# Performance work log

Hardware: AMD Instinct MI355X
Metric: run time of the kernel (lower is better)

The kernel has to match this reference:

```python
import jax, jax.numpy as jnp
import numpy as np

N, K, B, D, H = 256, 128, 256, 256, 512  # code length, info bits, batch, embed dim, MLP hidden


def _mlp(x, W1, b1, W2, b2):
    return jnp.maximum(x @ W1 + b1, 0.0) @ W2 + b2


def setup_inputs():
    key = jax.random.key(0)
    ks = jax.random.split(key, 12)
    perm = np.random.RandomState(0).permutation(N)
    info_set = jnp.sort(jnp.asarray(perm[:K], dtype=jnp.int32))  # unique sorted info positions
    info_bits = jax.random.randint(ks[0], (B, K), 0, 2, dtype=jnp.int32)
    rv = jax.random.uniform(ks[1], (B, N), dtype=jnp.float32)  # one uniform per leaf (sampling)

    def w(k, shape, fan):
        return jax.random.normal(k, shape, jnp.float32) / np.float32(np.sqrt(fan))

    return {
        'info_bits': info_bits,
        'rv': rv,
        'info_set': info_set,
        'obs_emb': w(ks[2], (3, D), D),
        'label_emb': w(ks[3], (3, D), D),
        'cn_W1': w(ks[4], (2 * D, H), 2 * D), 'cn_b1': jnp.zeros((H,), jnp.float32),
        'cn_W2': w(ks[5], (H, D), H), 'cn_b2': jnp.zeros((D,), jnp.float32),
        'bn_W1': w(ks[6], (3 * D, H), 3 * D), 'bn_b1': jnp.zeros((H,), jnp.float32),
        'bn_W2': w(ks[7], (H, D), H), 'bn_b2': jnp.zeros((D,), jnp.float32),
        'llr_W': w(ks[8], (D, 2), D), 'llr_b': jnp.zeros((2,), jnp.float32),
    }


def reference(info_bits, rv, info_set, obs_emb, label_emb,
              cn_W1, cn_b1, cn_W2, cn_b2, bn_W1, bn_b1, bn_W2, bn_b2, llr_W, llr_b):
    batch = info_bits.shape[0]

    def encode(e, f, off, n):
        # e: (B, n, D) float embeddings; f: (B, n, 1) int32 bits (2 == unknown -> sample)
        if n == 1:
            p_uy = jax.nn.softmax(e @ llr_W + llr_b, axis=-1)        # (B, 1, 2) probs
            r = rv[:, off:off + 1]                                    # (B, 1)
            # rv > cdf[...,0] == rv > p(u=0): sample a hard bit
            hard = (r > p_uy[..., 0]).astype(jnp.int32)[..., None]    # (B, 1, 1)
            x = jnp.where(f == 2, hard, f)
            return x, x, p_uy
        half = n // 2
        e_odd, e_even = e[:, ::2], e[:, 1::2]                         # SplitEvenOdd(axis=1)
        f_left, f_right = f[:, :half], f[:, half:]
        u1est = _mlp(jnp.concatenate([e_odd, e_even], -1), cn_W1, cn_b1, cn_W2, cn_b2)
        u1, h1, p_left = encode(u1est, f_left, off, half)
        u_emb = label_emb[h1[..., 0]]                                 # (B, half, D)
        u2est = _mlp(jnp.concatenate([e_odd, e_even, u_emb], -1), bn_W1, bn_b1, bn_W2, bn_b2)
        u2, h2, p_right = encode(u2est, f_right, off + half, half)
        u = jnp.concatenate([u1, u2], 1)
        p_uy = jnp.concatenate([p_left, p_right], 1)
        v_xor = jnp.mod(h1 + h2, 2)
        # Interleave(axis=1): out[::2] = v_xor, out[1::2] = h2
        x = jnp.stack([v_xor, h2], axis=2).reshape(batch, n, 1)
        return u, x, p_uy

    # scatter info bits into the length-N frame (frozen positions stay == 2)
    u_ = jnp.full((batch, N), 2, jnp.int32).at[:, info_set].set(info_bits)
    f = u_[..., None]
    # embedding_observations_nn(2 * ones): embedding of token '2' everywhere
    e = jnp.broadcast_to(obs_emb[2], (batch, N, D))
    u, x, p_u = encode(e, f, 0, N)
    # f: sampled frame with info positions re-masked to 2
    f_out = u[..., 0].at[:, info_set].set(2)[..., None]
    return x, f_out, u, p_u
```

## Files before the change

kernel.cpp:

```cpp
#include <hip/hip_runtime.h>
#include <math.h>

#define NB 256
#define NN 256
#define NK 128
#define ND 256
#define NH 512
#define NT 1024

#define OUT_X 0
#define OUT_F 65536
#define OUT_U 131072
#define OUT_P 196608

#define EPB   65280
#define SP6O  EPB
#define S1O   (SP6O + 1024)
#define S2O   (S1O + 512)
#define S3O   (S2O + 1024)
#define LOFFI (S3O + 2048)
#define BPB   (LOFFI + 256)

__host__ __device__ __forceinline__ int loff(int d) { return 256 - (1 << (9 - d)); }

template <int PC>
__device__ void g1ks(const float* __restrict__ Abuf, float* __restrict__ part,
                     const int tid, const float* __restrict__ W1) {
  const int q = tid >> 8;
  const int c0 = (tid & 255) << 1;
  const float* Wp = W1 + (size_t)(q * 128) * NH + c0;
  const float* Ar = Abuf + q * 128;
  float a0[PC], a1[PC];
#pragma unroll
  for (int r = 0; r < PC; ++r) { a0[r] = 0.f; a1[r] = 0.f; }
  float2 n0 = *(const float2*)Wp;
  float2 n1 = *(const float2*)(Wp + NH);
  float2 n2 = *(const float2*)(Wp + 2 * NH);
  float2 n3 = *(const float2*)(Wp + 3 * NH);
#pragma unroll 2
  for (int kc = 0; kc < 124; kc += 4) {
    const float2 w0 = n0, w1 = n1, w2 = n2, w3 = n3;
    const float* Wn = Wp + (size_t)(kc + 4) * NH;
    n0 = *(const float2*)Wn;
    n1 = *(const float2*)(Wn + NH);
    n2 = *(const float2*)(Wn + 2 * NH);
    n3 = *(const float2*)(Wn + 3 * NH);
#pragma unroll
    for (int r = 0; r < PC; ++r) {
      const float4 av = *(const float4*)(Ar + r * 512 + kc);
      a0[r] += av.x * w0.x + av.y * w1.x + av.z * w2.x + av.w * w3.x;
      a1[r] += av.x * w0.y + av.y * w1.y + av.z * w2.y + av.w * w3.y;
    }
  }
#pragma unroll
  for (int r = 0; r < PC; ++r) {
    const float4 av = *(const float4*)(Ar + r * 512 + 124);
    a0[r] += av.x * n0.x + av.y * n1.x + av.z * n2.x + av.w * n3.x;
    a1[r] += av.x * n0.y + av.y * n1.y + av.z * n2.y + av.w * n3.y;
  }
#pragma unroll
  for (int r = 0; r < PC; ++r)
    *(float2*)&part[(q * PC + r) * 512 + c0] = make_float2(a0[r], a1[r]);
}

template <int PC>
__device__ void g1red(const float* __restrict__ part, float* __restrict__ hid,
                      const int tid, const float* __restrict__ b1,
                      const int isBn, const float* __restrict__ embS,
                      const int* __restrict__ bitR) {
  for (int i = tid; i < PC * 256; i += NT) {
    const int r = i >> 8, c0 = (i & 255) << 1;
    float2 s = *(const float2*)(b1 + c0);
#pragma unroll
    for (int qq = 0; qq < 4; ++qq) {
      const float2 p = *(const float2*)&part[(qq * PC + r) * 512 + c0];
      s.x += p.x; s.y += p.y;
    }
    if (isBn) {
      const float2 e = *(const float2*)&embS[bitR[r] * 512 + c0];
      s.x += e.x; s.y += e.y;
    }
    *(float2*)&hid[r * 512 + c0] = make_float2(fmaxf(s.x, 0.f), fmaxf(s.y, 0.f));
  }
}

template <int R>
__device__ void g1redspec(const float* __restrict__ part, float* __restrict__ hid,
                          const int base, const int tid,
                          const float* __restrict__ b1,
                          const float* __restrict__ embS) {
  for (int i = tid; i < R * 256; i += NT) {
    const int r = i >> 8, c0 = (i & 255) << 1;
    float2 s = *(const float2*)(b1 + c0);
#pragma unroll
    for (int qq = 0; qq < 4; ++qq) {
      const float2 p = *(const float2*)&part[(qq * R + r) * 512 + c0];
      s.x += p.x; s.y += p.y;
    }
    const float2 e0 = *(const float2*)&embS[c0];
    const float2 e1 = *(const float2*)&embS[512 + c0];
    *(float2*)&hid[(base + 2 * r) * 512 + c0] =
        make_float2(fmaxf(s.x + e0.x, 0.f), fmaxf(s.y + e0.y, 0.f));
    *(float2*)&hid[(base + 2 * r + 1) * 512 + c0] =
        make_float2(fmaxf(s.x + e1.x, 0.f), fmaxf(s.y + e1.y, 0.f));
  }
}

template <int RT>
__device__ void g2ks(const float* __restrict__ hid, const int hidBase,
                     float* __restrict__ part, const int tid,
                     const float* __restrict__ W2) {
  const int q = tid >> 7;
  const int c0 = (tid & 127) << 1;
  const float* Wp = W2 + (size_t)(q * 64) * ND + c0;
  const float* Hr = hid + hidBase * 512 + q * 64;
  float a0[RT], a1[RT];
#pragma unroll
  for (int r = 0; r < RT; ++r) { a0[r] = 0.f; a1[r] = 0.f; }
  float2 n0 = *(const float2*)Wp;
  float2 n1 = *(const float2*)(Wp + ND);
  float2 n2 = *(const float2*)(Wp + 2 * ND);
  float2 n3 = *(const float2*)(Wp + 3 * ND);
#pragma unroll 2
  for (int kc = 0; kc < 60; kc += 4) {
    const float2 w0 = n0, w1 = n1, w2 = n2, w3 = n3;
    const float* Wn = Wp + (size_t)(kc + 4) * ND;
    n0 = *(const float2*)Wn;
    n1 = *(const float2*)(Wn + ND);
    n2 = *(const float2*)(Wn + 2 * ND);
    n3 = *(const float2*)(Wn + 3 * ND);
#pragma unroll
    for (int r = 0; r < RT; ++r) {
      const float4 av = *(const float4*)(Hr + r * 512 + kc);
      a0[r] += av.x * w0.x + av.y * w1.x + av.z * w2.x + av.w * w3.x;
      a1[r] += av.x * w0.y + av.y * w1.y + av.z * w2.y + av.w * w3.y;
    }
  }
#pragma unroll
  for (int r = 0; r < RT; ++r) {
    const float4 av = *(const float4*)(Hr + r * 512 + 60);
    a0[r] += av.x * n0.x + av.y * n1.x + av.z * n2.x + av.w * n3.x;
    a1[r] += av.x * n0.y + av.y * n1.y + av.z * n2.y + av.w * n3.y;
  }
#pragma unroll
  for (int r = 0; r < RT; ++r)
    *(float2*)&part[(q * RT + r) * 256 + c0] = make_float2(a0[r], a1[r]);
}

template <int RT>
__device__ void g2red(const float* __restrict__ part, const int tid,
                      const float* __restrict__ b2,
                      float* const* __restrict__ rowDst) {
  for (int i = tid; i < RT * 128; i += NT) {
    const int r = i >> 7, c0 = (i & 127) << 1;
    float2 s = *(const float2*)(b2 + c0);
#pragma unroll
    for (int qq = 0; qq < 8; ++qq) {
      const float2 p = *(const float2*)&part[(qq * RT + r) * 256 + c0];
      s.x += p.x; s.y += p.y;
    }
    *(float2*)(rowDst[r] + c0) = s;
  }
}

__global__ __launch_bounds__(NT, 4) void sc_quad(
    const int* __restrict__ info_bits, const float* __restrict__ rv,
    const int* __restrict__ info_set,
    const float* __restrict__ obs_emb, const float* __restrict__ label_emb,
    const float* __restrict__ cnW1, const float* __restrict__ cnb1,
    const float* __restrict__ cnW2, const float* __restrict__ cnb2,
    const float* __restrict__ bnW1, const float* __restrict__ bnb1,
    const float* __restrict__ bnW2, const float* __restrict__ bnb2,
    const float* __restrict__ llrW, const float* __restrict__ llrb,
    float* __restrict__ out, float* __restrict__ ws) {
  __shared__ float A[4096];
  __shared__ float part[20480];
  __shared__ float hid[8192];
  __shared__ float embS[1024];
  __shared__ float* rowDst[16];
  __shared__ int fmap[256];
  __shared__ int curS[256], nxtS[256];
  __shared__ float red[8];
  __shared__ int bitR[8];
  __shared__ int qbS[4];

  const int tid = threadIdx.x, b = blockIdx.x;
  float* wsb = ws + (size_t)b * BPB;
  float* E = wsb;
  float* sp6 = wsb + SP6O;
  float* S1 = wsb + S1O;
  float* S2 = wsb + S2O;
  float* S3 = wsb + S3O;
  int* Lb = (int*)(wsb + LOFFI);
  const float* obs2 = obs_emb + 2 * ND;

  {
    const int bit = tid >> 9, col = tid & 511;
    float s = 0.f;
#pragma unroll 4
    for (int j = 0; j < ND; ++j)
      s += label_emb[bit * ND + j] * bnW1[(size_t)(NH + j) * NH + col];
    embS[bit * 512 + col] = s;
  }
  if (tid < 256) fmap[tid] = -1;
  __syncthreads();
  if (tid < NK) fmap[info_set[tid]] = tid;
  __syncthreads();

  auto stageA = [&](const float* Ed, int p0, int R) {
    const int n4 = R * 128;
    float4* A4 = (float4*)A;
    if (Ed) {
      const float4* s4 = (const float4*)(Ed + (size_t)(2 * p0) * ND);
      for (int i = tid; i < n4; i += NT) A4[i] = s4[i];
    } else {
      const float4* o4 = (const float4*)obs2;
      for (int i = tid; i < n4; i += NT) A4[i] = o4[i & 63];
    }
  };

  auto plainPass = [&](int d, int isBn) {
    const int P = 1 << (7 - d);
    const float* W1 = isBn ? bnW1 : cnW1;
    const float* B1 = isBn ? bnb1 : cnb1;
    const float* W2 = isBn ? bnW2 : cnW2;
    const float* B2 = isBn ? bnb2 : cnb2;
    const float* Ed = (d == 0) ? nullptr : E + (size_t)loff(d) * ND;
    float* dstE = E + (size_t)loff(d + 1) * ND;
    const int PC = P >= 8 ? 8 : 4;
    for (int p0 = 0; p0 < P; p0 += PC) {
      stageA(Ed, p0, PC);
      if (isBn && tid < PC) bitR[tid] = Lb[loff(d + 1) + p0 + tid];
      if (tid < PC) rowDst[tid] = dstE + (size_t)(p0 + tid) * ND;
      __syncthreads();
      if (PC == 8) {
        g1ks<8>(A, part, tid, W1); __syncthreads();
        g1red<8>(part, hid, tid, B1, isBn, embS, bitR); __syncthreads();
        g2ks<8>(hid, 0, part, tid, W2); __syncthreads();
        g2red<8>(part, tid, B2, rowDst); __syncthreads();
      } else {
        g1ks<4>(A, part, tid, W1); __syncthreads();
        g1red<4>(part, hid, tid, B1, isBn, embS, bitR); __syncthreads();
        g2ks<4>(hid, 0, part, tid, W2); __syncthreads();
        g2red<4>(part, tid, B2, rowDst); __syncthreads();
      }
    }
  };

  auto pair6 = [&]() {
    stageA(E + (size_t)loff(6) * ND, 0, 2);
    if (tid < 2) rowDst[tid] = E + (size_t)(252 + tid) * ND;
    __syncthreads();
    g1ks<2>(A, part, tid, cnW1); __syncthreads();
    g1red<2>(part, hid, tid, cnb1, 0, embS, bitR); __syncthreads();
    g2ks<2>(hid, 0, part, tid, cnW2); __syncthreads();
    g2red<2>(part, tid, cnb2, rowDst); __syncthreads();
    g1ks<2>(A, part, tid, bnW1); __syncthreads();
    g1redspec<2>(part, hid, 2, tid, bnb1, embS); __syncthreads();
    g2ks<4>(hid, 2, part, tid, bnW2);
    if (tid < 4) rowDst[tid] = sp6 + (size_t)tid * ND;
    __syncthreads();
    g2red<4>(part, tid, bnb2, rowDst); __syncthreads();
  };

  auto comb = [&]() {
    for (int i = tid; i < 5 * 128; i += NT) {
      const int r = i >> 7, k = (i & 127) << 2;
      const int h = k >> 8;
      const float* src;
      if (r == 0) src = E + (size_t)(252 + h) * ND;
      else {
        const int cc = r - 1;
        const int bit = (h == 0) ? (cc >> 1) : (cc & 1);
        src = sp6 + (size_t)(h * 2 + bit) * ND;
      }
      *(float4*)&A[r * 512 + k] = *(const float4*)&src[k & 255];
    }
    __syncthreads();
    g1ks<5>(A, part, tid, cnW1); __syncthreads();
    g1red<5>(part, hid, tid, cnb1, 0, embS, bitR); __syncthreads();
    g2ks<5>(hid, 0, part, tid, cnW2);
    if (tid < 5) rowDst[tid] = (tid == 0) ? (E + (size_t)254 * ND)
                                          : (S2 + (size_t)(tid - 1) * ND);
    __syncthreads();
    g2red<5>(part, tid, cnb2, rowDst); __syncthreads();
    g1ks<5>(A, part, tid, bnW1); __syncthreads();
    g1redspec<5>(part, hid, 5, tid, bnb1, embS); __syncthreads();
    g2ks<10>(hid, 5, part, tid, bnW2);
    if (tid < 10) rowDst[tid] = (tid < 2) ? (S1 + (size_t)tid * ND)
                                          : (S3 + (size_t)(tid - 2) * ND);
    __syncthreads();
    g2red<10>(part, tid, bnb2, rowDst); __syncthreads();
  };

  auto leaf = [&](int off) {
    const int ph = off & 3;
    const float* src;
    if (ph == 0) src = E + (size_t)254 * ND;
    else if (ph == 1) src = S1 + (size_t)qbS[0] * ND;
    else {
      const int cidx = 2 * (qbS[0] ^ qbS[1]) + qbS[1];
      src = (ph == 2) ? (S2 + (size_t)cidx * ND)
                      : (S3 + (size_t)(2 * cidx + qbS[2]) * ND);
    }
    if (tid < 256) {
      const float ev = src[tid];
      float v0 = ev * llrW[2 * tid];
      float v1 = ev * llrW[2 * tid + 1];
#pragma unroll
      for (int o = 32; o > 0; o >>= 1) {
        v0 += __shfl_down(v0, o);
        v1 += __shfl_down(v1, o);
      }
      if ((tid & 63) == 0) {
        red[tid >> 6] = v0;
        red[4 + (tid >> 6)] = v1;
      }
    }
    __syncthreads();
    if (tid == 0) {
      const float l0 = red[0] + red[1] + red[2] + red[3] + llrb[0];
      const float l1 = red[4] + red[5] + red[6] + red[7] + llrb[1];
      const float m = fmaxf(l0, l1);
      const float e0 = expf(l0 - m), e1 = expf(l1 - m);
      const float s = e0 + e1;
      const float p0 = e0 / s, p1 = e1 / s;
      const int hard = (rv[b * NN + off] > p0) ? 1 : 0;
      const int fidx = fmap[off];
      const int fval = (fidx >= 0) ? info_bits[b * NK + fidx] : 2;
      const int xb = (fval == 2) ? hard : fval;
      out[OUT_F + b * NN + off] = (fidx >= 0) ? 2.0f : (float)xb;
      out[OUT_U + b * NN + off] = (float)xb;
      out[OUT_P + (b * NN + off) * 2 + 0] = p0;
      out[OUT_P + (b * NN + off) * 2 + 1] = p1;
      curS[0] = xb;
      qbS[ph] = xb;
    }
    __syncthreads();
    int* cur = curS;
    int* nxt = nxtS;
    int len = 1, lev = 8, idx = off;
    while (idx & 1) {
      if (tid < len) {
        const int c = cur[tid];
        nxt[2 * tid] = Lb[loff(lev) + tid] ^ c;
        nxt[2 * tid + 1] = c;
      }
      __syncthreads();
      int* t = cur; cur = nxt; nxt = t;
      len <<= 1; idx >>= 1; --lev;
    }
    if (lev > 0) {
      if (tid < len) Lb[loff(lev) + tid] = cur[tid];
    } else {
      if (tid < 256) out[OUT_X + b * NN + tid] = (float)cur[tid];
    }
    __syncthreads();
  };

  for (int d = 0; d <= 5; ++d) plainPass(d, 0);
  pair6();
  comb();

  for (int off = 0; off < NN; ++off) {
    leaf(off);
    if (off == NN - 1) break;
    const int t = off + 1;
    const int z = __ffs(t) - 1;
    if (z <= 1) continue;
    const int dbn = 7 - z;
    plainPass(dbn, 1);
    for (int d = dbn + 1; d <= 5; ++d) plainPass(d, 0);
    pair6();
    comb();
  }
}

extern "C" void kernel_launch(void* const* d_in, const int* in_sizes, int n_in,
                              void* d_out, int out_size, void* d_ws, size_t ws_size,
                              hipStream_t stream) {
  const int*   info_bits = (const int*)d_in[0];
  const float* rv        = (const float*)d_in[1];
  const int*   info_set  = (const int*)d_in[2];
  const float* obs_emb   = (const float*)d_in[3];
  const float* label_emb = (const float*)d_in[4];
  const float* cnW1      = (const float*)d_in[5];
  const float* cnb1      = (const float*)d_in[6];
  const float* cnW2      = (const float*)d_in[7];
  const float* cnb2      = (const float*)d_in[8];
  const float* bnW1      = (const float*)d_in[9];
  const float* bnb1      = (const float*)d_in[10];
  const float* bnW2      = (const float*)d_in[11];
  const float* bnb2      = (const float*)d_in[12];
  const float* llrW      = (const float*)d_in[13];
  const float* llrb      = (const float*)d_in[14];

  float* out = (float*)d_out;
  float* ws  = (float*)d_ws;

  sc_quad<<<dim3(NB), dim3(NT), 0, stream>>>(
      info_bits, rv, info_set, obs_emb, label_emb,
      cnW1, cnb1, cnW2, cnb2, bnW1, bnb1, bnW2, bnb2,
      llrW, llrb, out, ws);
}
```

Baseline: 13.35 ms.

## Add float4 K-split GEMV kernels and compute uniform first passes once

```diff
diff --git a/kernel.cpp b/kernel.cpp
--- a/kernel.cpp
+++ b/kernel.cpp
@@ -63,49 +63,6 @@
     *(float2*)&part[(q * PC + r) * 512 + c0] = make_float2(a0[r], a1[r]);
 }
 
-template <int PC>
-__device__ void g1red(const float* __restrict__ part, float* __restrict__ hid,
-                      const int tid, const float* __restrict__ b1,
-                      const int isBn, const float* __restrict__ embS,
-                      const int* __restrict__ bitR) {
-  for (int i = tid; i < PC * 256; i += NT) {
-    const int r = i >> 8, c0 = (i & 255) << 1;
-    float2 s = *(const float2*)(b1 + c0);
-#pragma unroll
-    for (int qq = 0; qq < 4; ++qq) {
-      const float2 p = *(const float2*)&part[(qq * PC + r) * 512 + c0];
-      s.x += p.x; s.y += p.y;
-    }
-    if (isBn) {
-      const float2 e = *(const float2*)&embS[bitR[r] * 512 + c0];
-      s.x += e.x; s.y += e.y;
-    }
-    *(float2*)&hid[r * 512 + c0] = make_float2(fmaxf(s.x, 0.f), fmaxf(s.y, 0.f));
-  }
-}
-
-template <int R>
-__device__ void g1redspec(const float* __restrict__ part, float* __restrict__ hid,
-                          const int base, const int tid,
-                          const float* __restrict__ b1,
-                          const float* __restrict__ embS) {
-  for (int i = tid; i < R * 256; i += NT) {
-    const int r = i >> 8, c0 = (i & 255) << 1;
-    float2 s = *(const float2*)(b1 + c0);
-#pragma unroll
-    for (int qq = 0; qq < 4; ++qq) {
-      const float2 p = *(const float2*)&part[(qq * R + r) * 512 + c0];
-      s.x += p.x; s.y += p.y;
-    }
-    const float2 e0 = *(const float2*)&embS[c0];
-    const float2 e1 = *(const float2*)&embS[512 + c0];
-    *(float2*)&hid[(base + 2 * r) * 512 + c0] =
-        make_float2(fmaxf(s.x + e0.x, 0.f), fmaxf(s.y + e0.y, 0.f));
-    *(float2*)&hid[(base + 2 * r + 1) * 512 + c0] =
-        make_float2(fmaxf(s.x + e1.x, 0.f), fmaxf(s.y + e1.y, 0.f));
-  }
-}
-
 template <int RT>
 __device__ void g2ks(const float* __restrict__ hid, const int hidBase,
                      float* __restrict__ part, const int tid,
@@ -147,7 +104,139 @@
     *(float2*)&part[(q * RT + r) * 256 + c0] = make_float2(a0[r], a1[r]);
 }
 
+template <int PC>
+__device__ void g1q(const float* __restrict__ Abuf, float* __restrict__ part,
+                    const int tid, const float* __restrict__ W1) {
+  const int q = tid >> 7;
+  const int c0 = (tid & 127) << 2;
+  const float* Wp = W1 + (size_t)(q * 64) * NH + c0;
+  const float* Ar = Abuf + q * 64;
+  float a0[PC], a1[PC], a2[PC], a3[PC];
+#pragma unroll
+  for (int r = 0; r < PC; ++r) { a0[r] = 0.f; a1[r] = 0.f; a2[r] = 0.f; a3[r] = 0.f; }
+  float4 n0 = *(const float4*)Wp;
+  float4 n1 = *(const float4*)(Wp + NH);
+  float4 n2 = *(const float4*)(Wp + 2 * NH);
+  float4 n3 = *(const float4*)(Wp + 3 * NH);
+#pragma unroll 2
+  for (int kc = 0; kc < 60; kc += 4) {
+    const float4 w0 = n0, w1 = n1, w2 = n2, w3 = n3;
+    const float* Wn = Wp + (size_t)(kc + 4) * NH;
+    n0 = *(const float4*)Wn;
+    n1 = *(const float4*)(Wn + NH);
+    n2 = *(const float4*)(Wn + 2 * NH);
+    n3 = *(const float4*)(Wn + 3 * NH);
+#pragma unroll
+    for (int r = 0; r < PC; ++r) {
+      const float4 av = *(const float4*)(Ar + r * 512 + kc);
+      a0[r] += av.x * w0.x + av.y * w1.x + av.z * w2.x + av.w * w3.x;
+      a1[r] += av.x * w0.y + av.y * w1.y + av.z * w2.y + av.w * w3.y;
+      a2[r] += av.x * w0.z + av.y * w1.z + av.z * w2.z + av.w * w3.z;
+      a3[r] += av.x * w0.w + av.y * w1.w + av.z * w2.w + av.w * w3.w;
+    }
+  }
+#pragma unroll
+  for (int r = 0; r < PC; ++r) {
+    const float4 av = *(const float4*)(Ar + r * 512 + 60);
+    a0[r] += av.x * n0.x + av.y * n1.x + av.z * n2.x + av.w * n3.x;
+    a1[r] += av.x * n0.y + av.y * n1.y + av.z * n2.y + av.w * n3.y;
+    a2[r] += av.x * n0.z + av.y * n1.z + av.z * n2.z + av.w * n3.z;
+    a3[r] += av.x * n0.w + av.y * n1.w + av.z * n2.w + av.w * n3.w;
+  }
+#pragma unroll
+  for (int r = 0; r < PC; ++r)
+    *(float4*)&part[(q * PC + r) * 512 + c0] = make_float4(a0[r], a1[r], a2[r], a3[r]);
+}
+
 template <int RT>
+__device__ void g2q(const float* __restrict__ hid, const int hidBase,
+                    float* __restrict__ part, const int tid,
+                    const float* __restrict__ W2) {
+  const int q = tid >> 6;
+  const int c0 = (tid & 63) << 2;
+  const float* Wp = W2 + (size_t)(q * 32) * ND + c0;
+  const float* Hr = hid + hidBase * 512 + q * 32;
+  float a0[RT], a1[RT], a2[RT], a3[RT];
+#pragma unroll
+  for (int r = 0; r < RT; ++r) { a0[r] = 0.f; a1[r] = 0.f; a2[r] = 0.f; a3[r] = 0.f; }
+  float4 n0 = *(const float4*)Wp;
+  float4 n1 = *(const float4*)(Wp + ND);
+  float4 n2 = *(const float4*)(Wp + 2 * ND);
+  float4 n3 = *(const float4*)(Wp + 3 * ND);
+#pragma unroll 2
+  for (int kc = 0; kc < 28; kc += 4) {
+    const float4 w0 = n0, w1 = n1, w2 = n2, w3 = n3;
+    const float* Wn = Wp + (size_t)(kc + 4) * ND;
+    n0 = *(const float4*)Wn;
+    n1 = *(const float4*)(Wn + ND);
+    n2 = *(const float4*)(Wn + 2 * ND);
+    n3 = *(const float4*)(Wn + 3 * ND);
+#pragma unroll
+    for (int r = 0; r < RT; ++r) {
+      const float4 av = *(const float4*)(Hr + r * 512 + kc);
+      a0[r] += av.x * w0.x + av.y * w1.x + av.z * w2.x + av.w * w3.x;
+      a1[r] += av.x * w0.y + av.y * w1.y + av.z * w2.y + av.w * w3.y;
+      a2[r] += av.x * w0.z + av.y * w1.z + av.z * w2.z + av.w * w3.z;
+      a3[r] += av.x * w0.w + av.y * w1.w + av.z * w2.w + av.w * w3.w;
+    }
+  }
+#pragma unroll
+  for (int r = 0; r < RT; ++r) {
+    const float4 av = *(const float4*)(Hr + r * 512 + 28);
+    a0[r] += av.x * n0.x + av.y * n1.x + av.z * n2.x + av.w * n3.x;
+    a1[r] += av.x * n0.y + av.y * n1.y + av.z * n2.y + av.w * n3.y;
+    a2[r] += av.x * n0.z + av.y * n1.z + av.z * n2.z + av.w * n3.z;
+    a3[r] += av.x * n0.w + av.y * n1.w + av.z * n2.w + av.w * n3.w;
+  }
+#pragma unroll
+  for (int r = 0; r < RT; ++r)
+    *(float4*)&part[(q * RT + r) * 256 + c0] = make_float4(a0[r], a1[r], a2[r], a3[r]);
+}
+
+template <int KS, int PC>
+__device__ void g1red(const float* __restrict__ part, float* __restrict__ hid,
+                      const int tid, const float* __restrict__ b1,
+                      const int isBn, const float* __restrict__ embS,
+                      const int* __restrict__ bitR) {
+  for (int i = tid; i < PC * 256; i += NT) {
+    const int r = i >> 8, c0 = (i & 255) << 1;
+    float2 s = *(const float2*)(b1 + c0);
+#pragma unroll
+    for (int qq = 0; qq < KS; ++qq) {
+      const float2 p = *(const float2*)&part[(qq * PC + r) * 512 + c0];
+      s.x += p.x; s.y += p.y;
+    }
+    if (isBn) {
+      const float2 e = *(const float2*)&embS[bitR[r] * 512 + c0];
+      s.x += e.x; s.y += e.y;
+    }
+    *(float2*)&hid[r * 512 + c0] = make_float2(fmaxf(s.x, 0.f), fmaxf(s.y, 0.f));
+  }
+}
+
+template <int KS, int R>
+__device__ void g1redspec(const float* __restrict__ part, float* __restrict__ hid,
+                          const int base, const int tid,
+                          const float* __restrict__ b1,
+                          const float* __restrict__ embS) {
+  for (int i = tid; i < R * 256; i += NT) {
+    const int r = i >> 8, c0 = (i & 255) << 1;
+    float2 s = *(const float2*)(b1 + c0);
+#pragma unroll
+    for (int qq = 0; qq < KS; ++qq) {
+      const float2 p = *(const float2*)&part[(qq * R + r) * 512 + c0];
+      s.x += p.x; s.y += p.y;
+    }
+    const float2 e0 = *(const float2*)&embS[c0];
+    const float2 e1 = *(const float2*)&embS[512 + c0];
+    *(float2*)&hid[(base + 2 * r) * 512 + c0] =
+        make_float2(fmaxf(s.x + e0.x, 0.f), fmaxf(s.y + e0.y, 0.f));
+    *(float2*)&hid[(base + 2 * r + 1) * 512 + c0] =
+        make_float2(fmaxf(s.x + e1.x, 0.f), fmaxf(s.y + e1.y, 0.f));
+  }
+}
+
+template <int KS, int RT>
 __device__ void g2red(const float* __restrict__ part, const int tid,
                       const float* __restrict__ b2,
                       float* const* __restrict__ rowDst) {
@@ -155,7 +244,7 @@
     const int r = i >> 7, c0 = (i & 127) << 1;
     float2 s = *(const float2*)(b2 + c0);
 #pragma unroll
-    for (int qq = 0; qq < 8; ++qq) {
+    for (int qq = 0; qq < KS; ++qq) {
       const float2 p = *(const float2*)&part[(qq * RT + r) * 256 + c0];
       s.x += p.x; s.y += p.y;
     }
@@ -177,6 +266,7 @@
   __shared__ float part[20480];
   __shared__ float hid[8192];
   __shared__ float embS[1024];
+  __shared__ float rowBuf[256];
   __shared__ float* rowDst[16];
   __shared__ int fmap[256];
   __shared__ int curS[256], nxtS[256];
@@ -235,32 +325,47 @@
       __syncthreads();
       if (PC == 8) {
         g1ks<8>(A, part, tid, W1); __syncthreads();
-        g1red<8>(part, hid, tid, B1, isBn, embS, bitR); __syncthreads();
+        g1red<4, 8>(part, hid, tid, B1, isBn, embS, bitR); __syncthreads();
         g2ks<8>(hid, 0, part, tid, W2); __syncthreads();
-        g2red<8>(part, tid, B2, rowDst); __syncthreads();
+        g2red<8, 8>(part, tid, B2, rowDst); __syncthreads();
       } else {
-        g1ks<4>(A, part, tid, W1); __syncthreads();
-        g1red<4>(part, hid, tid, B1, isBn, embS, bitR); __syncthreads();
-        g2ks<4>(hid, 0, part, tid, W2); __syncthreads();
-        g2red<4>(part, tid, B2, rowDst); __syncthreads();
+        g1q<4>(A, part, tid, W1); __syncthreads();
+        g1red<8, 4>(part, hid, tid, B1, isBn, embS, bitR); __syncthreads();
+        g2q<4>(hid, 0, part, tid, W2); __syncthreads();
+        g2red<16, 4>(part, tid, B2, rowDst); __syncthreads();
       }
     }
+  };
+
+  auto uniPass = [&](int d) {
+    const int P = 1 << (7 - d);
+    const float* Ed = (d == 0) ? nullptr : E + (size_t)loff(d) * ND;
+    float* dstE = E + (size_t)loff(d + 1) * ND;
+    stageA(Ed, 0, 1);
+    if (tid == 0) rowDst[0] = rowBuf;
+    __syncthreads();
+    g1q<1>(A, part, tid, cnW1); __syncthreads();
+    g1red<8, 1>(part, hid, tid, cnb1, 0, embS, bitR); __syncthreads();
+    g2q<1>(hid, 0, part, tid, cnW2); __syncthreads();
+    g2red<16, 1>(part, tid, cnb2, rowDst); __syncthreads();
+    for (int i = tid; i < P * 256; i += NT) dstE[i] = rowBuf[i & 255];
+    __syncthreads();
   };
 
   auto pair6 = [&]() {
     stageA(E + (size_t)loff(6) * ND, 0, 2);
     if (tid < 2) rowDst[tid] = E + (size_t)(252 + tid) * ND;
     __syncthreads();
-    g1ks<2>(A, part, tid, cnW1); __syncthreads();
-    g1red<2>(part, hid, tid, cnb1, 0, embS, bitR); __syncthreads();
-    g2ks<2>(hid, 0, part, tid, cnW2); __syncthreads();
-    g2red<2>(part, tid, cnb2, rowDst); __syncthreads();
-    g1ks<2>(A, part, tid, bnW1); __syncthreads();
-    g1redspec<2>(part, hid, 2, tid, bnb1, embS); __syncthreads();
-    g2ks<4>(hid, 2, part, tid, bnW2);
+    g1q<2>(A, part, tid, cnW1); __syncthreads();
+    g1red<8, 2>(part, hid, tid, cnb1, 0, embS, bitR); __syncthreads();
+    g2q<2>(hid, 0, part, tid, cnW2); __syncthreads();
+    g2red<16, 2>(part, tid, cnb2, rowDst); __syncthreads();
+    g1q<2>(A, part, tid, bnW1); __syncthreads();
+    g1redspec<8, 2>(part, hid, 2, tid, bnb1, embS); __syncthreads();
+    g2q<4>(hid, 2, part, tid, bnW2);
     if (tid < 4) rowDst[tid] = sp6 + (size_t)tid * ND;
     __syncthreads();
-    g2red<4>(part, tid, bnb2, rowDst); __syncthreads();
+    g2red<16, 4>(part, tid, bnb2, rowDst); __syncthreads();
   };
 
   auto comb = [&]() {
@@ -277,20 +382,20 @@
       *(float4*)&A[r * 512 + k] = *(const float4*)&src[k & 255];
     }
     __syncthreads();
-    g1ks<5>(A, part, tid, cnW1); __syncthreads();
-    g1red<5>(part, hid, tid, cnb1, 0, embS, bitR); __syncthreads();
-    g2ks<5>(hid, 0, part, tid, cnW2);
+    g1q<5>(A, part, tid, cnW1); __syncthreads();
+    g1red<8, 5>(part, hid, tid, cnb1, 0, embS, bitR); __syncthreads();
+    g2q<5>(hid, 0, part, tid, cnW2);
     if (tid < 5) rowDst[tid] = (tid == 0) ? (E + (size_t)254 * ND)
                                           : (S2 + (size_t)(tid - 1) * ND);
     __syncthreads();
-    g2red<5>(part, tid, cnb2, rowDst); __syncthreads();
-    g1ks<5>(A, part, tid, bnW1); __syncthreads();
-    g1redspec<5>(part, hid, 5, tid, bnb1, embS); __syncthreads();
+    g2red<16, 5>(part, tid, cnb2, rowDst); __syncthreads();
+    g1q<5>(A, part, tid, bnW1); __syncthreads();
+    g1redspec<8, 5>(part, hid, 5, tid, bnb1, embS); __syncthreads();
     g2ks<10>(hid, 5, part, tid, bnW2);
     if (tid < 10) rowDst[tid] = (tid < 2) ? (S1 + (size_t)tid * ND)
                                           : (S3 + (size_t)(tid - 2) * ND);
     __syncthreads();
-    g2red<10>(part, tid, bnb2, rowDst); __syncthreads();
+    g2red<8, 10>(part, tid, bnb2, rowDst); __syncthreads();
   };
 
   auto leaf = [&](int off) {
@@ -358,7 +463,7 @@
     __syncthreads();
   };
 
-  for (int d = 0; d <= 5; ++d) plainPass(d, 0);
+  for (int d = 0; d <= 5; ++d) uniPass(d);
   pair6();
   comb();
 
```

Result: faster. 10.80 ms (median of 2 runs) (-19.1%).

## Stage W1 tiles in LDS with double buffering and dedupe uniform prefix passes

Applied to the files above, without the earlier changes.

```diff
diff --git a/kernel.cpp b/kernel.cpp
--- a/kernel.cpp
+++ b/kernel.cpp
@@ -23,87 +23,73 @@
 
 __host__ __device__ __forceinline__ int loff(int d) { return 256 - (1 << (9 - d)); }
 
-template <int PC>
-__device__ void g1ks(const float* __restrict__ Abuf, float* __restrict__ part,
-                     const int tid, const float* __restrict__ W1) {
-  const int q = tid >> 8;
-  const int c0 = (tid & 255) << 1;
-  const float* Wp = W1 + (size_t)(q * 128) * NH + c0;
-  const float* Ar = Abuf + q * 128;
-  float a0[PC], a1[PC];
-#pragma unroll
-  for (int r = 0; r < PC; ++r) { a0[r] = 0.f; a1[r] = 0.f; }
-  float2 n0 = *(const float2*)Wp;
-  float2 n1 = *(const float2*)(Wp + NH);
-  float2 n2 = *(const float2*)(Wp + 2 * NH);
-  float2 n3 = *(const float2*)(Wp + 3 * NH);
-#pragma unroll 2
-  for (int kc = 0; kc < 124; kc += 4) {
-    const float2 w0 = n0, w1 = n1, w2 = n2, w3 = n3;
-    const float* Wn = Wp + (size_t)(kc + 4) * NH;
-    n0 = *(const float2*)Wn;
-    n1 = *(const float2*)(Wn + NH);
-    n2 = *(const float2*)(Wn + 2 * NH);
-    n3 = *(const float2*)(Wn + 3 * NH);
-#pragma unroll
-    for (int r = 0; r < PC; ++r) {
-      const float4 av = *(const float4*)(Ar + r * 512 + kc);
-      a0[r] += av.x * w0.x + av.y * w1.x + av.z * w2.x + av.w * w3.x;
-      a1[r] += av.x * w0.y + av.y * w1.y + av.z * w2.y + av.w * w3.y;
-    }
-  }
-#pragma unroll
-  for (int r = 0; r < PC; ++r) {
-    const float4 av = *(const float4*)(Ar + r * 512 + 124);
-    a0[r] += av.x * n0.x + av.y * n1.x + av.z * n2.x + av.w * n3.x;
-    a1[r] += av.x * n0.y + av.y * n1.y + av.z * n2.y + av.w * n3.y;
-  }
-#pragma unroll
-  for (int r = 0; r < PC; ++r)
-    *(float2*)&part[(q * PC + r) * 512 + c0] = make_float2(a0[r], a1[r]);
-}
-
-template <int PC>
-__device__ void g1red(const float* __restrict__ part, float* __restrict__ hid,
-                      const int tid, const float* __restrict__ b1,
-                      const int isBn, const float* __restrict__ embS,
-                      const int* __restrict__ bitR) {
-  for (int i = tid; i < PC * 256; i += NT) {
-    const int r = i >> 8, c0 = (i & 255) << 1;
-    float2 s = *(const float2*)(b1 + c0);
-#pragma unroll
-    for (int qq = 0; qq < 4; ++qq) {
-      const float2 p = *(const float2*)&part[(qq * PC + r) * 512 + c0];
-      s.x += p.x; s.y += p.y;
-    }
-    if (isBn) {
-      const float2 e = *(const float2*)&embS[bitR[r] * 512 + c0];
-      s.x += e.x; s.y += e.y;
-    }
-    *(float2*)&hid[r * 512 + c0] = make_float2(fmaxf(s.x, 0.f), fmaxf(s.y, 0.f));
-  }
-}
-
-template <int R>
-__device__ void g1redspec(const float* __restrict__ part, float* __restrict__ hid,
-                          const int base, const int tid,
-                          const float* __restrict__ b1,
-                          const float* __restrict__ embS) {
-  for (int i = tid; i < R * 256; i += NT) {
-    const int r = i >> 8, c0 = (i & 255) << 1;
-    float2 s = *(const float2*)(b1 + c0);
-#pragma unroll
-    for (int qq = 0; qq < 4; ++qq) {
-      const float2 p = *(const float2*)&part[(qq * R + r) * 512 + c0];
-      s.x += p.x; s.y += p.y;
-    }
-    const float2 e0 = *(const float2*)&embS[c0];
-    const float2 e1 = *(const float2*)&embS[512 + c0];
-    *(float2*)&hid[(base + 2 * r) * 512 + c0] =
-        make_float2(fmaxf(s.x + e0.x, 0.f), fmaxf(s.y + e0.y, 0.f));
-    *(float2*)&hid[(base + 2 * r + 1) * 512 + c0] =
-        make_float2(fmaxf(s.x + e1.x, 0.f), fmaxf(s.y + e1.y, 0.f));
-  }
+template <int R, int MODE>
+__device__ void g1lds(const float* __restrict__ A, float* __restrict__ wbuf,
+                      float* __restrict__ hid, const int hidBase, const int tid,
+                      const float* __restrict__ W1, const float* __restrict__ b1,
+                      const float* __restrict__ embS, const int* __restrict__ bitR) {
+  constexpr int RPT = (R + 1) / 2;
+  const int c = tid & 511;
+  const int rg = tid >> 9;
+  const int r0 = rg * RPT;
+  float acc[RPT];
+#pragma unroll
+  for (int i = 0; i < RPT; ++i) acc[i] = 0.f;
+  {
+    const float4* src = (const float4*)W1;
+    const float4 v0 = src[tid * 2];
+    const float4 v1 = src[tid * 2 + 1];
+    *(float4*)&wbuf[tid * 8] = v0;
+    *(float4*)&wbuf[tid * 8 + 4] = v1;
+  }
+  for (int kt = 0; kt < 32; ++kt) {
+    __syncthreads();
+    float4 n0 = make_float4(0.f, 0.f, 0.f, 0.f);
+    float4 n1 = make_float4(0.f, 0.f, 0.f, 0.f);
+    if (kt < 31) {
+      const float4* src = (const float4*)(W1 + (kt + 1) * 8192);
+      n0 = src[tid * 2];
+      n1 = src[tid * 2 + 1];
+    }
+    const float* wt = wbuf + (kt & 1) * 8192;
+    const int k0 = kt * 16;
+#pragma unroll
+    for (int kq = 0; kq < 4; ++kq) {
+      const float w0 = wt[(kq * 4 + 0) * 512 + c];
+      const float w1 = wt[(kq * 4 + 1) * 512 + c];
+      const float w2 = wt[(kq * 4 + 2) * 512 + c];
+      const float w3 = wt[(kq * 4 + 3) * 512 + c];
+#pragma unroll
+      for (int i = 0; i < RPT; ++i) {
+        const int r = r0 + i;
+        if (r < R) {
+          const float4 av = *(const float4*)&A[r * 512 + k0 + kq * 4];
+          acc[i] += av.x * w0 + av.y * w1 + av.z * w2 + av.w * w3;
+        }
+      }
+    }
+    if (kt < 31) {
+      float* wn = wbuf + ((kt + 1) & 1) * 8192;
+      *(float4*)&wn[tid * 8] = n0;
+      *(float4*)&wn[tid * 8 + 4] = n1;
+    }
+  }
+#pragma unroll
+  for (int i = 0; i < RPT; ++i) {
+    const int r = r0 + i;
+    if (r < R) {
+      const float pre = acc[i] + b1[c];
+      if (MODE == 0) {
+        hid[(hidBase + r) * 512 + c] = fmaxf(pre, 0.f);
+      } else if (MODE == 1) {
+        hid[(hidBase + r) * 512 + c] = fmaxf(pre + embS[bitR[r] * 512 + c], 0.f);
+      } else {
+        hid[(hidBase + 2 * r) * 512 + c] = fmaxf(pre + embS[c], 0.f);
+        hid[(hidBase + 2 * r + 1) * 512 + c] = fmaxf(pre + embS[512 + c], 0.f);
+      }
+    }
+  }
+  __syncthreads();
 }
 
 template <int RT>
@@ -148,6 +134,51 @@
 }
 
 template <int RT>
+__device__ void g2q(const float* __restrict__ hid, const int hidBase,
+                    float* __restrict__ part, const int tid,
+                    const float* __restrict__ W2) {
+  const int q = tid >> 6;
+  const int c0 = (tid & 63) << 2;
+  const float* Wp = W2 + (size_t)(q * 32) * ND + c0;
+  const float* Hr = hid + hidBase * 512 + q * 32;
+  float a0[RT], a1[RT], a2[RT], a3[RT];
+#pragma unroll
+  for (int r = 0; r < RT; ++r) { a0[r] = 0.f; a1[r] = 0.f; a2[r] = 0.f; a3[r] = 0.f; }
+  float4 n0 = *(const float4*)Wp;
+  float4 n1 = *(const float4*)(Wp + ND);
+  float4 n2 = *(const float4*)(Wp + 2 * ND);
+  float4 n3 = *(const float4*)(Wp + 3 * ND);
+#pragma unroll 2
+  for (int kc = 0; kc < 28; kc += 4) {
+    const float4 w0 = n0, w1 = n1, w2 = n2, w3 = n3;
+    const float* Wn = Wp + (size_t)(kc + 4) * ND;
+    n0 = *(const float4*)Wn;
+    n1 = *(const float4*)(Wn + ND);
+    n2 = *(const float4*)(Wn + 2 * ND);
+    n3 = *(const float4*)(Wn + 3 * ND);
+#pragma unroll
+    for (int r = 0; r < RT; ++r) {
+      const float4 av = *(const float4*)(Hr + r * 512 + kc);
+      a0[r] += av.x * w0.x + av.y * w1.x + av.z * w2.x + av.w * w3.x;
+      a1[r] += av.x * w0.y + av.y * w1.y + av.z * w2.y + av.w * w3.y;
+      a2[r] += av.x * w0.z + av.y * w1.z + av.z * w2.z + av.w * w3.z;
+      a3[r] += av.x * w0.w + av.y * w1.w + av.z * w2.w + av.w * w3.w;
+    }
+  }
+#pragma unroll
+  for (int r = 0; r < RT; ++r) {
+    const float4 av = *(const float4*)(Hr + r * 512 + 28);
+    a0[r] += av.x * n0.x + av.y * n1.x + av.z * n2.x + av.w * n3.x;
+    a1[r] += av.x * n0.y + av.y * n1.y + av.z * n2.y + av.w * n3.y;
+    a2[r] += av.x * n0.z + av.y * n1.z + av.z * n2.z + av.w * n3.z;
+    a3[r] += av.x * n0.w + av.y * n1.w + av.z * n2.w + av.w * n3.w;
+  }
+#pragma unroll
+  for (int r = 0; r < RT; ++r)
+    *(float4*)&part[(q * RT + r) * 256 + c0] = make_float4(a0[r], a1[r], a2[r], a3[r]);
+}
+
+template <int KS, int RT>
 __device__ void g2red(const float* __restrict__ part, const int tid,
                       const float* __restrict__ b2,
                       float* const* __restrict__ rowDst) {
@@ -155,7 +186,7 @@
     const int r = i >> 7, c0 = (i & 127) << 1;
     float2 s = *(const float2*)(b2 + c0);
 #pragma unroll
-    for (int qq = 0; qq < 8; ++qq) {
+    for (int qq = 0; qq < KS; ++qq) {
       const float2 p = *(const float2*)&part[(qq * RT + r) * 256 + c0];
       s.x += p.x; s.y += p.y;
     }
@@ -163,7 +194,7 @@
   }
 }
 
-__global__ __launch_bounds__(NT, 4) void sc_quad(
+__global__ __launch_bounds__(NT, 4) void sc_v14(
     const int* __restrict__ info_bits, const float* __restrict__ rv,
     const int* __restrict__ info_set,
     const float* __restrict__ obs_emb, const float* __restrict__ label_emb,
@@ -173,10 +204,11 @@
     const float* __restrict__ bnW2, const float* __restrict__ bnb2,
     const float* __restrict__ llrW, const float* __restrict__ llrb,
     float* __restrict__ out, float* __restrict__ ws) {
+  __shared__ float scrU[20480];
   __shared__ float A[4096];
-  __shared__ float part[20480];
-  __shared__ float hid[8192];
+  __shared__ float hid[7680];
   __shared__ float embS[1024];
+  __shared__ float rowBuf[256];
   __shared__ float* rowDst[16];
   __shared__ int fmap[256];
   __shared__ int curS[256], nxtS[256];
@@ -232,35 +264,44 @@
       stageA(Ed, p0, PC);
       if (isBn && tid < PC) bitR[tid] = Lb[loff(d + 1) + p0 + tid];
       if (tid < PC) rowDst[tid] = dstE + (size_t)(p0 + tid) * ND;
-      __syncthreads();
       if (PC == 8) {
-        g1ks<8>(A, part, tid, W1); __syncthreads();
-        g1red<8>(part, hid, tid, B1, isBn, embS, bitR); __syncthreads();
-        g2ks<8>(hid, 0, part, tid, W2); __syncthreads();
-        g2red<8>(part, tid, B2, rowDst); __syncthreads();
+        if (isBn) g1lds<8, 1>(A, scrU, hid, 0, tid, W1, B1, embS, bitR);
+        else      g1lds<8, 0>(A, scrU, hid, 0, tid, W1, B1, embS, bitR);
+        g2ks<8>(hid, 0, scrU, tid, W2); __syncthreads();
+        g2red<8, 8>(scrU, tid, B2, rowDst); __syncthreads();
       } else {
-        g1ks<4>(A, part, tid, W1); __syncthreads();
-        g1red<4>(part, hid, tid, B1, isBn, embS, bitR); __syncthreads();
-        g2ks<4>(hid, 0, part, tid, W2); __syncthreads();
-        g2red<4>(part, tid, B2, rowDst); __syncthreads();
-      }
-    }
+        if (isBn) g1lds<4, 1>(A, scrU, hid, 0, tid, W1, B1, embS, bitR);
+        else      g1lds<4, 0>(A, scrU, hid, 0, tid, W1, B1, embS, bitR);
+        g2q<4>(hid, 0, scrU, tid, W2); __syncthreads();
+        g2red<16, 4>(scrU, tid, B2, rowDst); __syncthreads();
+      }
+    }
+  };
+
+  auto uniPass = [&](int d) {
+    const int P = 1 << (7 - d);
+    const float* Ed = (d == 0) ? nullptr : E + (size_t)loff(d) * ND;
+    float* dstE = E + (size_t)loff(d + 1) * ND;
+    stageA(Ed, 0, 1);
+    if (tid == 0) rowDst[0] = rowBuf;
+    g1lds<1, 0>(A, scrU, hid, 0, tid, cnW1, cnb1, embS, bitR);
+    g2q<1>(hid, 0, scrU, tid, cnW2); __syncthreads();
+    g2red<16, 1>(scrU, tid, cnb2, rowDst); __syncthreads();
+    for (int i = tid; i < P * 256; i += NT) dstE[i] = rowBuf[i & 255];
+    __syncthreads();
   };
 
   auto pair6 = [&]() {
     stageA(E + (size_t)loff(6) * ND, 0, 2);
     if (tid < 2) rowDst[tid] = E + (size_t)(252 + tid) * ND;
-    __syncthreads();
-    g1ks<2>(A, part, tid, cnW1); __syncthreads();
-    g1red<2>(part, hid, tid, cnb1, 0, embS, bitR); __syncthreads();
-    g2ks<2>(hid, 0, part, tid, cnW2); __syncthreads();
-    g2red<2>(part, tid, cnb2, rowDst); __syncthreads();
-    g1ks<2>(A, part, tid, bnW1); __syncthreads();
-    g1redspec<2>(part, hid, 2, tid, bnb1, embS); __syncthreads();
-    g2ks<4>(hid, 2, part, tid, bnW2);
+    g1lds<2, 0>(A, scrU, hid, 0, tid, cnW1, cnb1, embS, bitR);
+    g2q<2>(hid, 0, scrU, tid, cnW2); __syncthreads();
+    g2red<16, 2>(scrU, tid, cnb2, rowDst); __syncthreads();
+    g1lds<2, 2>(A, scrU, hid, 2, tid, bnW1, bnb1, embS, bitR);
+    g2ks<4>(hid, 2, scrU, tid, bnW2);
     if (tid < 4) rowDst[tid] = sp6 + (size_t)tid * ND;
     __syncthreads();
-    g2red<4>(part, tid, bnb2, rowDst); __syncthreads();
+    g2red<8, 4>(scrU, tid, bnb2, rowDst); __syncthreads();
   };
 
   auto comb = [&]() {
@@ -276,21 +317,18 @@
       }
       *(float4*)&A[r * 512 + k] = *(const float4*)&src[k & 255];
     }
-    __syncthreads();
-    g1ks<5>(A, part, tid, cnW1); __syncthreads();
-    g1red<5>(part, hid, tid, cnb1, 0, embS, bitR); __syncthreads();
-    g2ks<5>(hid, 0, part, tid, cnW2);
+    g1lds<5, 0>(A, scrU, hid, 0, tid, cnW1, cnb1, embS, bitR);
+    g2ks<5>(hid, 0, scrU, tid, cnW2);
     if (tid < 5) rowDst[tid] = (tid == 0) ? (E + (size_t)254 * ND)
                                           : (S2 + (size_t)(tid - 1) * ND);
     __syncthreads();
-    g2red<5>(part, tid, cnb2, rowDst); __syncthreads();
-    g1ks<5>(A, part, tid, bnW1); __syncthreads();
-    g1redspec<5>(part, hid, 5, tid, bnb1, embS); __syncthreads();
-    g2ks<10>(hid, 5, part, tid, bnW2);
+    g2red<8, 5>(scrU, tid, cnb2, rowDst); __syncthreads();
+    g1lds<5, 2>(A, scrU, hid, 5, tid, bnW1, bnb1, embS, bitR);
+    g2ks<10>(hid, 5, scrU, tid, bnW2);
     if (tid < 10) rowDst[tid] = (tid < 2) ? (S1 + (size_t)tid * ND)
                                           : (S3 + (size_t)(tid - 2) * ND);
     __syncthreads();
-    g2red<10>(part, tid, bnb2, rowDst); __syncthreads();
+    g2red<8, 10>(scrU, tid, bnb2, rowDst); __syncthreads();
   };
 
   auto leaf = [&](int off) {
@@ -358,7 +396,7 @@
     __syncthreads();
   };
 
-  for (int d = 0; d <= 5; ++d) plainPass(d, 0);
+  for (int d = 0; d <= 5; ++d) uniPass(d);
   pair6();
   comb();
 
@@ -398,7 +436,7 @@
   float* out = (float*)d_out;
   float* ws  = (float*)d_ws;
 
-  sc_quad<<<dim3(NB), dim3(NT), 0, stream>>>(
+  sc_v14<<<dim3(NB), dim3(NT), 0, stream>>>(
       info_bits, rv, info_set, obs_emb, label_emb,
       cnW1, cnb1, cnW2, cnb2, bnW1, bnb1, bnW2, bnb2,
       llrW, llrb, out, ws);
```

After: 18.55 ms. 38.9% more time.
